# Performance work log

Hardware: AMD Instinct MI355X
Metric: run time of the kernel (lower is better)

Reference implementation:

```python
import jax, jax.numpy as jnp
import numpy as np

N_NODES = 50000
N_EDGES = 1600000
N_PAIRS = 2000000
N_GRAPHS = 50
HEADS = 4
HID = 32
T_LIMIT = 1.0
NEG_SLOPE = 0.2
LN_EPS = 1e-5


def setup_inputs() -> dict:
    key = jax.random.key(0)
    ks = jax.random.split(key, 24)
    inp = {}
    inp['x'] = jax.random.normal(ks[0], (N_NODES, 128), jnp.float32)
    inp['t'] = jax.random.uniform(ks[1], (N_NODES,), jnp.float32)
    inp['edge_index'] = jax.random.randint(ks[2], (2, N_EDGES), 0, N_NODES, jnp.int32)
    inp['pair_index'] = jax.random.randint(ks[3], (2, N_PAIRS), 0, N_NODES, jnp.int32)
    inp['batch'] = jnp.sort(jax.random.randint(ks[4], (N_NODES,), 0, N_GRAPHS, jnp.int32))
    s = lambda *sh: 0.05
    inp['t_W'] = jax.random.normal(ks[5], (3, 256), jnp.float32) * 0.3
    inp['t_b'] = jax.random.normal(ks[6], (256,), jnp.float32) * 0.05
    inp['W0_l'] = jax.random.normal(ks[7], (384, HEADS * HID), jnp.float32) * 0.05
    inp['b0_l'] = jax.random.normal(ks[8], (HEADS * HID,), jnp.float32) * 0.05
    inp['W0_r'] = jax.random.normal(ks[9], (384, HEADS * HID), jnp.float32) * 0.05
    inp['b0_r'] = jax.random.normal(ks[10], (HEADS * HID,), jnp.float32) * 0.05
    inp['att0'] = jax.random.normal(ks[11], (HEADS, HID), jnp.float32) * 0.1
    inp['bias0'] = jax.random.normal(ks[12], (HEADS * HID,), jnp.float32) * 0.05
    inp['Wl'] = jax.random.normal(ks[13], (3, HEADS * HID, HEADS * HID), jnp.float32) * 0.08
    inp['bl'] = jax.random.normal(ks[14], (3, HEADS * HID), jnp.float32) * 0.05
    inp['Wr'] = jax.random.normal(ks[15], (3, HEADS * HID, HEADS * HID), jnp.float32) * 0.08
    inp['br'] = jax.random.normal(ks[16], (3, HEADS * HID), jnp.float32) * 0.05
    inp['att'] = jax.random.normal(ks[17], (3, HEADS, HID), jnp.float32) * 0.1
    inp['bias'] = jax.random.normal(ks[18], (3, HEADS * HID), jnp.float32) * 0.05
    inp['ln_w'] = jnp.ones((4, HEADS * HID), jnp.float32)
    inp['ln_b'] = jnp.zeros((4, HEADS * HID), jnp.float32)
    inp['link_W'] = jax.random.normal(ks[19], (HEADS * HID, 1), jnp.float32) * 0.1
    inp['link_b'] = jnp.zeros((1,), jnp.float32)
    return inp


def gatv2_layer(h, src, dst, Wl_, bl_, Wr_, br_, att_, bias_):
    # GATv2Conv (concat heads, add_self_loops already folded into src/dst)
    n = h.shape[0]
    xl = (h @ Wl_ + bl_).reshape(n, HEADS, HID)   # source transform
    xr = (h @ Wr_ + br_).reshape(n, HEADS, HID)   # target transform
    m = jax.nn.leaky_relu(xl[src] + xr[dst], NEG_SLOPE)      # [E,H,C]
    logits = jnp.einsum('ehc,hc->eh', m, att_)               # [E,H]
    lmax = jax.ops.segment_max(logits, dst, num_segments=n)
    lmax = jnp.where(jnp.isfinite(lmax), lmax, 0.0)
    e = jnp.exp(logits - lmax[dst])
    denom = jax.ops.segment_sum(e, dst, num_segments=n)
    alpha = e / (denom[dst] + 1e-16)                         # scatter-softmax
    out = jax.ops.segment_sum(alpha[:, :, None] * xl[src], dst, num_segments=n)
    return out.reshape(n, HEADS * HID) + bias_


def graph_layernorm(h, batch, w, b):
    # PyG LayerNorm, mode='graph': normalize over all nodes+channels per graph
    n, f = h.shape
    cnt = jax.ops.segment_sum(jnp.ones((n,), h.dtype), batch, num_segments=N_GRAPHS) * f
    cnt = jnp.maximum(cnt, 1.0)
    mean = jax.ops.segment_sum(h.sum(axis=1), batch, num_segments=N_GRAPHS) / cnt
    hc = h - mean[batch][:, None]
    var = jax.ops.segment_sum((hc * hc).sum(axis=1), batch, num_segments=N_GRAPHS) / cnt
    return hc / jnp.sqrt(var + LN_EPS)[batch][:, None] * w + b


def reference(x, t, edge_index, pair_index, batch, t_W, t_b, W0_l, b0_l, W0_r, b0_r,
              att0, bias0, Wl, bl, Wr, br, att, bias, ln_w, ln_b, link_W, link_b):
    n = x.shape[0]
    # time embedding MLP with swish
    ta = (t / T_LIMIT)[:, None]
    feats = jnp.concatenate([jnp.sin(ta * (np.pi / 2)), jnp.cos(ta * (np.pi / 2)), ta], axis=1)
    te = feats @ t_W + t_b
    te = te * jax.nn.sigmoid(te)
    h = jnp.concatenate([x, te], axis=1)  # [N, 384]
    # self loops (added by GATv2Conv each layer)
    loops = jnp.arange(n, dtype=edge_index.dtype)
    src = jnp.concatenate([edge_index[0], loops])
    dst = jnp.concatenate([edge_index[1], loops])
    h = gatv2_layer(h, src, dst, W0_l, b0_l, W0_r, b0_r, att0, bias0)
    h = graph_layernorm(h, batch, ln_w[0], ln_b[0])
    for i in range(3):
        h = gatv2_layer(h, src, dst, Wl[i], bl[i], Wr[i], br[i], att[i], bias[i])
        h = graph_layernorm(h, batch, ln_w[i + 1], ln_b[i + 1])
    # edge-gather link scoring
    prod = h[pair_index[0]] * h[pair_index[1]]          # [E_pairs, 128]
    return jax.nn.sigmoid(prod @ link_W + link_b)[:, 0]
```

## Files before the change

kernel.cpp:

```cpp
#include <hip/hip_runtime.h>
#include <hip/hip_bf16.h>
#include <hip/hip_fp16.h>

#define N_NODES 50000
#define N_EDGES 1600000
#define E_TOT   1650000
#define N_PAIRS 2000000
#define N_GRAPHS 50
#define SCAN_NB 196

typedef __attribute__((ext_vector_type(2))) _Float16 half2_t;
typedef __attribute__((ext_vector_type(4))) _Float16 half4_t;
typedef __attribute__((ext_vector_type(8))) _Float16 half8_t;
typedef __attribute__((ext_vector_type(4))) float floatx4;

union H8 { half8_t v; half2_t h2[4]; uint32_t u[4]; };

__global__ void k_time_embed(const float* __restrict__ x, const float* __restrict__ t,
                             const float* __restrict__ tW, const float* __restrict__ tb,
                             _Float16* __restrict__ h0h) {
    int i = blockIdx.x;
    int tid = threadIdx.x;
    float ta = t[i];
    float s = sinf(ta * 1.5707963267948966f);
    float c = cosf(ta * 1.5707963267948966f);
    if (tid < 128) h0h[(size_t)i*384 + tid] = (_Float16)x[(size_t)i*128 + tid];
    float v = s*tW[tid] + c*tW[256+tid] + ta*tW[512+tid] + tb[tid];
    float sw = v / (1.f + __expf(-v));
    h0h[(size_t)i*384 + 128 + tid] = (_Float16)sw;
}

__global__ void k_cvt_w(const float* __restrict__ Wl, const float* __restrict__ Wr,
                        const float* __restrict__ bl, const float* __restrict__ br,
                        int K, _Float16* __restrict__ WT, float* __restrict__ b2) {
    int idx = blockIdx.x*256 + threadIdx.x;
    if (idx < 256) b2[idx] = (idx < 128) ? bl[idx] : br[idx-128];
    if (idx >= 256*K) return;
    int n = idx / K, k = idx - n*K;
    float v = (n < 128) ? Wl[k*128 + n] : Wr[k*128 + (n-128)];
    WT[idx] = (_Float16)v;
}

__global__ void k_edge_hist(const int* __restrict__ ei, int* __restrict__ deg) {
    int e = blockIdx.x*256 + threadIdx.x;
    if (e >= E_TOT) return;
    int dst = (e < N_EDGES) ? ei[N_EDGES + e] : (e - N_EDGES);
    atomicAdd(&deg[dst], 1);
}

__global__ void k_goff(const int* __restrict__ batch, int* __restrict__ goff) {
    int i = blockIdx.x*256 + threadIdx.x;
    if (i >= N_NODES) return;
    int bi = batch[i];
    if (i == 0) {
        for (int g = 0; g <= bi; ++g) goff[g] = 0;
    } else {
        int bp = batch[i-1];
        for (int g = bp+1; g <= bi; ++g) goff[g] = i;
    }
    if (i == N_NODES-1) {
        for (int g = bi+1; g <= N_GRAPHS; ++g) goff[g] = N_NODES;
    }
}

__global__ void k_scan1(const int* __restrict__ deg, int* __restrict__ row_ptr,
                        int* __restrict__ bsums) {
    __shared__ int tmp[256];
    int tid = threadIdx.x;
    int i = blockIdx.x*256 + tid;
    int v = (i < N_NODES) ? deg[i] : 0;
    tmp[tid] = v; __syncthreads();
    for (int off = 1; off < 256; off <<= 1) {
        int tv = (tid >= off) ? tmp[tid-off] : 0;
        __syncthreads();
        tmp[tid] += tv;
        __syncthreads();
    }
    int inc = tmp[tid];
    if (i < N_NODES) row_ptr[i] = inc - v;
    if (tid == 255) bsums[blockIdx.x] = inc;
}

__global__ void k_scan2(int* __restrict__ bsums, int nb) {
    __shared__ int tmp[256];
    int tid = threadIdx.x;
    int v = (tid < nb) ? bsums[tid] : 0;
    tmp[tid] = v; __syncthreads();
    for (int off = 1; off < 256; off <<= 1) {
        int tv = (tid >= off) ? tmp[tid-off] : 0;
        __syncthreads();
        tmp[tid] += tv;
        __syncthreads();
    }
    bsums[tid] = tmp[tid] - v;
}

__global__ void k_scan3(int* __restrict__ row_ptr, const int* __restrict__ bsums,
                        int* __restrict__ cursor) {
    int i = blockIdx.x*256 + threadIdx.x;
    if (i < N_NODES) {
        int v = row_ptr[i] + bsums[blockIdx.x];
        row_ptr[i] = v;
        cursor[i] = v;
    }
    if (i == 0) row_ptr[N_NODES] = E_TOT;
}

__global__ void k_scatter(const int* __restrict__ ei, int* __restrict__ cursor,
                          int* __restrict__ csr_src) {
    int e = blockIdx.x*256 + threadIdx.x;
    if (e >= E_TOT) return;
    int src, dst;
    if (e < N_EDGES) { src = ei[e]; dst = ei[N_EDGES + e]; }
    else             { src = e - N_EDGES; dst = src; }
    int pos = atomicAdd(&cursor[dst], 1);
    csr_src[pos] = src;
}

template<int K>
__global__ __launch_bounds__(256) void k_gemm_mfma(
    const _Float16* __restrict__ Ah, const _Float16* __restrict__ WT,
    const float* __restrict__ b2,
    _Float16* __restrict__ xl_h, float* __restrict__ xr) {
    int wave = (blockIdx.x*256 + threadIdx.x) >> 6;
    int lane = threadIdx.x & 63;
    if (wave >= N_NODES/16) return;
    int m0 = wave * 16;
    int r16 = lane & 15, quad = lane >> 4;
    constexpr int KT = K / 32;
    half8_t afrag[KT];
    const _Float16* arow = Ah + (size_t)(m0 + r16)*K + quad*8;
    #pragma unroll
    for (int kt = 0; kt < KT; ++kt)
        afrag[kt] = *(const half8_t*)(arow + kt*32);
    #pragma unroll
    for (int nt = 0; nt < 16; ++nt) {
        floatx4 acc = {0.f, 0.f, 0.f, 0.f};
        const _Float16* brow = WT + (size_t)(nt*16 + r16)*K + quad*8;
        #pragma unroll
        for (int kt = 0; kt < KT; ++kt) {
            half8_t bfrag = *(const half8_t*)(brow + kt*32);
            acc = __builtin_amdgcn_mfma_f32_16x16x32_f16(afrag[kt], bfrag, acc, 0, 0, 0);
        }
        int col = nt*16 + r16;
        float bv = b2[col];
        if (nt < 8) {
            #pragma unroll
            for (int r = 0; r < 4; ++r)
                xl_h[(size_t)(m0 + quad*4 + r)*128 + col] = (_Float16)(acc[r] + bv);
        } else {
            #pragma unroll
            for (int r = 0; r < 4; ++r)
                xr[(size_t)(m0 + quad*4 + r)*128 + (col-128)] = acc[r] + bv;
        }
    }
}

__global__ __launch_bounds__(256) void k_gemm_ln_mfma(
    const float* __restrict__ hout, const int* __restrict__ batch,
    const int* __restrict__ goff, const float* __restrict__ gsum,
    const float* __restrict__ gsumsq, const float* __restrict__ lnw,
    const float* __restrict__ lnb, const _Float16* __restrict__ WT,
    const float* __restrict__ b2,
    _Float16* __restrict__ xl_h, float* __restrict__ xr) {
    int wave = (blockIdx.x*256 + threadIdx.x) >> 6;
    int lane = threadIdx.x & 63;
    if (wave >= N_NODES/16) return;
    int m0 = wave * 16;
    int r16 = lane & 15, quad = lane >> 4;
    int row = m0 + r16;
    int g = batch[row];
    float cnt = (float)(goff[g+1] - goff[g]) * 128.f;
    cnt = fmaxf(cnt, 1.f);
    float mean = gsum[g] / cnt;
    float var = gsumsq[g] / cnt - mean*mean;
    var = fmaxf(var, 0.f);
    float rstd = rsqrtf(var + 1e-5f);

    half8_t afrag[4];
    const float* arow = hout + (size_t)row*128 + quad*8;
    #pragma unroll
    for (int kt = 0; kt < 4; ++kt) {
        int c = quad*8 + kt*32;
        const float4* v4 = (const float4*)(arow + kt*32);
        const float4* w4 = (const float4*)(lnw + c);
        const float4* b4 = (const float4*)(lnb + c);
        float4 v0 = v4[0], v1 = v4[1];
        float4 w0 = w4[0], w1 = w4[1];
        float4 bb0 = b4[0], bb1 = b4[1];
        float vv[8] = {v0.x,v0.y,v0.z,v0.w,v1.x,v1.y,v1.z,v1.w};
        float ww[8] = {w0.x,w0.y,w0.z,w0.w,w1.x,w1.y,w1.z,w1.w};
        float bz[8] = {bb0.x,bb0.y,bb0.z,bb0.w,bb1.x,bb1.y,bb1.z,bb1.w};
        #pragma unroll
        for (int j = 0; j < 8; ++j)
            afrag[kt][j] = (_Float16)((vv[j] - mean) * rstd * ww[j] + bz[j]);
    }
    #pragma unroll
    for (int nt = 0; nt < 16; ++nt) {
        floatx4 acc = {0.f, 0.f, 0.f, 0.f};
        const _Float16* brow = WT + (size_t)(nt*16 + r16)*128 + quad*8;
        #pragma unroll
        for (int kt = 0; kt < 4; ++kt) {
            half8_t bfrag = *(const half8_t*)(brow + kt*32);
            acc = __builtin_amdgcn_mfma_f32_16x16x32_f16(afrag[kt], bfrag, acc, 0, 0, 0);
        }
        int col = nt*16 + r16;
        float bv = b2[col];
        if (nt < 8) {
            #pragma unroll
            for (int r = 0; r < 4; ++r)
                xl_h[(size_t)(m0 + quad*4 + r)*128 + col] = (_Float16)(acc[r] + bv);
        } else {
            #pragma unroll
            for (int r = 0; r < 4; ++r)
                xr[(size_t)(m0 + quad*4 + r)*128 + (col-128)] = acc[r] + bv;
        }
    }
}

__global__ __launch_bounds__(256) void k_gat(
    const _Float16* __restrict__ xl_h, const float* __restrict__ xr,
    const int* __restrict__ row_ptr, const int* __restrict__ csr_src,
    const float* __restrict__ att, const float* __restrict__ bias,
    float* __restrict__ hout, float2* __restrict__ nstats) {
    int wave = (blockIdx.x * 256 + threadIdx.x) >> 6;
    int lane = threadIdx.x & 63;
    if (wave >= N_NODES) return;
    int i = wave;
    int slot = lane >> 4;
    int l16  = lane & 15;
    int c0   = l16 * 8;

    H8 atth, xrh;
    {
        const float4* a4 = (const float4*)(att + c0);
        const float4* r4 = (const float4*)(xr + (size_t)i*128 + c0);
        float4 a0 = a4[0], a1 = a4[1], r0 = r4[0], r1 = r4[1];
        float af[8] = {a0.x,a0.y,a0.z,a0.w,a1.x,a1.y,a1.z,a1.w};
        float rf[8] = {r0.x,r0.y,r0.z,r0.w,r1.x,r1.y,r1.z,r1.w};
        #pragma unroll
        for (int j = 0; j < 8; ++j) {
            atth.v[j] = (_Float16)af[j];
            xrh.v[j]  = (_Float16)rf[j];
        }
    }
    int p0 = row_ptr[i], p1 = row_ptr[i+1];

    float denom = 0.f;
    float acc[8];
    #pragma unroll
    for (int j = 0; j < 8; ++j) acc[j] = 0.f;

    for (int p = p0; p < p1; p += 8) {
        int e1 = p + slot, e2 = p + 4 + slot;
        int i1 = csr_src[(e1 < p1) ? e1 : (p1 - 1)];
        int i2 = csr_src[(e2 < p1) ? e2 : (p1 - 1)];
        H8 g1, g2, m1, m2;
        g1.v = *(const half8_t*)(xl_h + (size_t)i1*128 + c0);
        g2.v = *(const half8_t*)(xl_h + (size_t)i2*128 + c0);
        m1.v = g1.v + xrh.v;
        m2.v = g2.v + xrh.v;
        float pa1 = 0.f, pb1 = 0.f, pa2 = 0.f, pb2 = 0.f;
        #pragma unroll
        for (int j = 0; j < 4; ++j) {
            half2_t ab1 = __builtin_bit_cast(half2_t, m1.u[j] & 0x7FFF7FFFu);
            half2_t ab2 = __builtin_bit_cast(half2_t, m2.u[j] & 0x7FFF7FFFu);
            pa1 = __builtin_amdgcn_fdot2(m1.h2[j], atth.h2[j], pa1, false);
            pb1 = __builtin_amdgcn_fdot2(ab1,      atth.h2[j], pb1, false);
            pa2 = __builtin_amdgcn_fdot2(m2.h2[j], atth.h2[j], pa2, false);
            pb2 = __builtin_amdgcn_fdot2(ab2,      atth.h2[j], pb2, false);
        }
        float pt1 = 0.6f*pa1 + 0.4f*pb1;
        float pt2 = 0.6f*pa2 + 0.4f*pb2;
        pt1 += __shfl_xor(pt1, 1);  pt2 += __shfl_xor(pt2, 1);
        pt1 += __shfl_xor(pt1, 2);  pt2 += __shfl_xor(pt2, 2);
        float w1 = (e1 < p1) ? __expf(pt1) : 0.f;
        float w2 = (e2 < p1) ? __expf(pt2) : 0.f;
        denom += w1 + w2;
        #pragma unroll
        for (int j = 0; j < 8; ++j) {
            acc[j] = fmaf(w1, (float)g1.v[j], acc[j]);
            acc[j] = fmaf(w2, (float)g2.v[j], acc[j]);
        }
    }
    #pragma unroll
    for (int off = 16; off <= 32; off <<= 1) {
        denom += __shfl_xor(denom, off);
        #pragma unroll
        for (int j = 0; j < 8; ++j) acc[j] += __shfl_xor(acc[j], off);
    }
    float inv = 1.f / (denom + 1e-16f);
    float v[8];
    float s1 = 0.f, s2 = 0.f;
    #pragma unroll
    for (int j = 0; j < 8; ++j) {
        v[j] = acc[j] * inv + bias[c0 + j];
        s1 += v[j];
        s2 = fmaf(v[j], v[j], s2);
    }
    if (slot == 0) {
        float4* o4 = (float4*)(hout + (size_t)i*128 + c0);
        o4[0] = make_float4(v[0], v[1], v[2], v[3]);
        o4[1] = make_float4(v[4], v[5], v[6], v[7]);
    }
    #pragma unroll
    for (int off = 1; off < 16; off <<= 1) {
        s1 += __shfl_xor(s1, off);
        s2 += __shfl_xor(s2, off);
    }
    if (lane == 0) nstats[i] = make_float2(s1, s2);
}

__global__ __launch_bounds__(256) void k_graph_red(
    const float2* __restrict__ nstats, const int* __restrict__ goff,
    float* __restrict__ gsum, float* __restrict__ gsumsq) {
    __shared__ float l1[256], l2[256];
    int g = blockIdx.x;
    int tid = threadIdx.x;
    int a = goff[g], b = goff[g+1];
    float s1 = 0.f, s2 = 0.f;
    for (int i = a + tid; i < b; i += 256) {
        float2 v = nstats[i];
        s1 += v.x; s2 += v.y;
    }
    l1[tid] = s1; l2[tid] = s2; __syncthreads();
    for (int off = 128; off > 0; off >>= 1) {
        if (tid < off) { l1[tid] += l1[tid+off]; l2[tid] += l2[tid+off]; }
        __syncthreads();
    }
    if (tid == 0) { gsum[g] = l1[0]; gsumsq[g] = l2[0]; }
}

__global__ void k_ln(const float* __restrict__ hout, const int* __restrict__ batch,
                     const int* __restrict__ goff, const float* __restrict__ gsum,
                     const float* __restrict__ gsumsq, const float* __restrict__ w,
                     const float* __restrict__ b, _Float16* __restrict__ hb) {
    int idx = blockIdx.x*256 + threadIdx.x;
    if (idx >= N_NODES*128) return;
    int i = idx >> 7, c = idx & 127;
    int g = batch[i];
    float cnt = (float)(goff[g+1] - goff[g]) * 128.f;
    cnt = fmaxf(cnt, 1.f);
    float mean = gsum[g] / cnt;
    float var = gsumsq[g] / cnt - mean*mean;
    var = fmaxf(var, 0.f);
    float rstd = rsqrtf(var + 1e-5f);
    float v = (hout[idx] - mean) * rstd * w[c] + b[c];
    hb[idx] = (_Float16)v;
}

__global__ __launch_bounds__(256) void k_pairs(
    const _Float16* __restrict__ hb, const int* __restrict__ pi,
    const float* __restrict__ lW, const float* __restrict__ lb,
    float* __restrict__ out) {
    int grp = (blockIdx.x*256 + threadIdx.x) >> 4;
    int q = threadIdx.x & 15;
    if (grp >= N_PAIRS) return;
    H8 w;
    #pragma unroll
    for (int j = 0; j < 8; ++j) w.v[j] = (_Float16)lW[q*8 + j];
    int p0 = pi[grp], p1 = pi[N_PAIRS + grp];
    const half8_t* B = (const half8_t*)hb;
    H8 a, b, prod;
    a.v = B[(size_t)p0*16 + q];
    b.v = B[(size_t)p1*16 + q];
    prod.v = a.v * b.v;
    float part = 0.f;
    #pragma unroll
    for (int j = 0; j < 4; ++j)
        part = __builtin_amdgcn_fdot2(prod.h2[j], w.h2[j], part, false);
    part += __shfl_xor(part, 1);
    part += __shfl_xor(part, 2);
    part += __shfl_xor(part, 4);
    part += __shfl_xor(part, 8);
    if (q == 0) out[grp] = 1.f / (1.f + __expf(-(part + lb[0])));
}

extern "C" void kernel_launch(void* const* d_in, const int* in_sizes, int n_in,
                              void* d_out, int out_size, void* d_ws, size_t ws_size,
                              hipStream_t stream) {
    const float* x     = (const float*)d_in[0];
    const float* t     = (const float*)d_in[1];
    const int*   ei    = (const int*)  d_in[2];
    const int*   pi    = (const int*)  d_in[3];
    const int*   batch = (const int*)  d_in[4];
    const float* tW    = (const float*)d_in[5];
    const float* tb    = (const float*)d_in[6];
    const float* W0l   = (const float*)d_in[7];
    const float* b0l   = (const float*)d_in[8];
    const float* W0r   = (const float*)d_in[9];
    const float* b0r   = (const float*)d_in[10];
    const float* att0  = (const float*)d_in[11];
    const float* bias0 = (const float*)d_in[12];
    const float* Wl    = (const float*)d_in[13];
    const float* bl    = (const float*)d_in[14];
    const float* Wr    = (const float*)d_in[15];
    const float* br    = (const float*)d_in[16];
    const float* att   = (const float*)d_in[17];
    const float* bias  = (const float*)d_in[18];
    const float* lnw   = (const float*)d_in[19];
    const float* lnb   = (const float*)d_in[20];
    const float* lW    = (const float*)d_in[21];
    const float* lb    = (const float*)d_in[22];
    float* out = (float*)d_out;

    char* ws = (char*)d_ws;
    size_t off = 0;
    auto walloc = [&](size_t bytes) -> void* {
        void* p = ws + off;
        off += (bytes + 255) & ~(size_t)255;
        return p;
    };
    _Float16*  h0h     = (_Float16*) walloc((size_t)N_NODES*384*2);
    float*     hout    = (float*)    walloc((size_t)N_NODES*128*4);
    _Float16*  xl_h    = (_Float16*) walloc((size_t)N_NODES*128*2);
    float*     xr      = (float*)    walloc((size_t)N_NODES*128*4);
    _Float16*  hb      = (_Float16*) walloc((size_t)N_NODES*128*2);
    int*       deg     = (int*)      walloc((size_t)N_NODES*4);
    int*       row_ptr = (int*)      walloc((size_t)(N_NODES+1)*4);
    int*       csr_src = (int*)      walloc((size_t)E_TOT*4);
    int*       bsums   = (int*)      walloc(256*4);
    int*       goff    = (int*)      walloc(64*4);
    float2*    nstats  = (float2*)   walloc((size_t)N_NODES*8);
    float*     stats   = (float*)    walloc(2*64*4);
    _Float16*  WT0     = (_Float16*) walloc(256*384*2);
    _Float16*  WT123   = (_Float16*) walloc(3*256*128*2);
    float*     b2      = (float*)    walloc(4*256*4);

    hipMemsetAsync(deg, 0, (size_t)N_NODES*4, stream);

    k_time_embed<<<N_NODES, 256, 0, stream>>>(x, t, tW, tb, h0h);
    k_cvt_w<<<(256*384+255)/256, 256, 0, stream>>>(W0l, W0r, b0l, b0r, 384, WT0, b2);
    for (int l = 0; l < 3; ++l)
        k_cvt_w<<<(256*128+255)/256, 256, 0, stream>>>(
            Wl + (size_t)l*128*128, Wr + (size_t)l*128*128,
            bl + l*128, br + l*128, 128, WT123 + (size_t)l*256*128, b2 + (l+1)*256);
    k_edge_hist<<<(E_TOT+255)/256, 256, 0, stream>>>(ei, deg);
    k_goff<<<SCAN_NB, 256, 0, stream>>>(batch, goff);
    k_scan1<<<SCAN_NB, 256, 0, stream>>>(deg, row_ptr, bsums);
    k_scan2<<<1, 256, 0, stream>>>(bsums, SCAN_NB);
    k_scan3<<<SCAN_NB, 256, 0, stream>>>(row_ptr, bsums, deg);
    k_scatter<<<(E_TOT+255)/256, 256, 0, stream>>>(ei, deg, csr_src);

    float* gsum   = stats;
    float* gsumsq = stats + 64;
    const int GEMM_BLOCKS = (N_NODES/16 + 3) / 4;
    for (int L = 0; L < 4; ++L) {
        if (L == 0)
            k_gemm_mfma<384><<<GEMM_BLOCKS, 256, 0, stream>>>(h0h, WT0, b2, xl_h, xr);
        else
            k_gemm_ln_mfma<<<GEMM_BLOCKS, 256, 0, stream>>>(
                hout, batch, goff, gsum, gsumsq, lnw + (L-1)*128, lnb + (L-1)*128,
                WT123 + (size_t)(L-1)*256*128, b2 + L*256, xl_h, xr);
        const float* attL  = (L == 0) ? att0  : att  + (size_t)(L-1)*128;
        const float* biasL = (L == 0) ? bias0 : bias + (size_t)(L-1)*128;
        k_gat<<<N_NODES/4, 256, 0, stream>>>(xl_h, xr, row_ptr, csr_src, attL, biasL,
                                             hout, nstats);
        k_graph_red<<<N_GRAPHS, 256, 0, stream>>>(nstats, goff, gsum, gsumsq);
    }
    k_ln<<<(N_NODES*128+255)/256, 256, 0, stream>>>(hout, batch, goff, gsum, gsumsq,
                                                    lnw + 3*128, lnb + 3*128, hb);
    k_pairs<<<((size_t)N_PAIRS*16 + 255)/256, 256, 0, stream>>>(hb, pi, lW, lb, out);
}
```

Baseline: 959.0 us.

## Replace global-atomic CSR build with two-pass bucketed scatter in shared memory

The CSR construction moves from a global per-node degree histogram plus scan plus global-atomic scatter to a two-level bucket sort. Edges are first binned into 256 buckets of 196 destination nodes using shared-memory histograms. A second pass sorts each bucket locally and writes row_ptr and csr_src with shared-memory atomics only. This is meant to cut global atomic contention and scattered writes, at the cost of an extra staging buffer and an additional read of the edge list. The packed stage word holds src in 16 bits, and source ids up to 49999 fit in that.

Result: faster. 821.3 us (-14.4%).

```diff
diff --git a/kernel.cpp b/kernel.cpp
--- a/kernel.cpp
+++ b/kernel.cpp
@@ -8,6 +8,9 @@
 #define N_PAIRS 2000000
 #define N_GRAPHS 50
 #define SCAN_NB 196
+#define NB2 256
+#define BSZ 196
+#define SCAT_BLOCKS 256
 
 typedef __attribute__((ext_vector_type(2))) _Float16 half2_t;
 typedef __attribute__((ext_vector_type(4))) _Float16 half4_t;
@@ -41,13 +44,6 @@
     WT[idx] = (_Float16)v;
 }
 
-__global__ void k_edge_hist(const int* __restrict__ ei, int* __restrict__ deg) {
-    int e = blockIdx.x*256 + threadIdx.x;
-    if (e >= E_TOT) return;
-    int dst = (e < N_EDGES) ? ei[N_EDGES + e] : (e - N_EDGES);
-    atomicAdd(&deg[dst], 1);
-}
-
 __global__ void k_goff(const int* __restrict__ batch, int* __restrict__ goff) {
     int i = blockIdx.x*256 + threadIdx.x;
     if (i >= N_NODES) return;
@@ -63,58 +59,105 @@
     }
 }
 
-__global__ void k_scan1(const int* __restrict__ deg, int* __restrict__ row_ptr,
-                        int* __restrict__ bsums) {
-    __shared__ int tmp[256];
+__global__ __launch_bounds__(256) void k_bhist(const int* __restrict__ ei,
+                                               int* __restrict__ bcnt) {
+    __shared__ int lh[NB2];
     int tid = threadIdx.x;
-    int i = blockIdx.x*256 + tid;
-    int v = (i < N_NODES) ? deg[i] : 0;
+    lh[tid] = 0;
+    __syncthreads();
+    int chunk = (E_TOT + gridDim.x - 1) / gridDim.x;
+    int e0 = blockIdx.x * chunk;
+    int e1 = min(e0 + chunk, E_TOT);
+    for (int e = e0 + tid; e < e1; e += 256) {
+        int dst = (e < N_EDGES) ? ei[N_EDGES + e] : (e - N_EDGES);
+        atomicAdd(&lh[dst / BSZ], 1);
+    }
+    __syncthreads();
+    if (lh[tid]) atomicAdd(&bcnt[tid], lh[tid]);
+}
+
+__global__ void k_bscan(const int* __restrict__ bcnt, int* __restrict__ bbase,
+                        int* __restrict__ bcursor) {
+    __shared__ int tmp[NB2];
+    int tid = threadIdx.x;
+    int v = bcnt[tid];
     tmp[tid] = v; __syncthreads();
-    for (int off = 1; off < 256; off <<= 1) {
-        int tv = (tid >= off) ? tmp[tid-off] : 0;
+    for (int off = 1; off < NB2; off <<= 1) {
+        int t = (tid >= off) ? tmp[tid-off] : 0;
         __syncthreads();
-        tmp[tid] += tv;
+        tmp[tid] += t;
         __syncthreads();
     }
-    int inc = tmp[tid];
-    if (i < N_NODES) row_ptr[i] = inc - v;
-    if (tid == 255) bsums[blockIdx.x] = inc;
-}
-
-__global__ void k_scan2(int* __restrict__ bsums, int nb) {
-    __shared__ int tmp[256];
+    int excl = tmp[tid] - v;
+    bbase[tid] = excl;
+    bcursor[tid] = excl;
+    if (tid == NB2-1) bbase[NB2] = tmp[tid];
+}
+
+__global__ __launch_bounds__(256) void k_scat1(const int* __restrict__ ei,
+                                               int* __restrict__ bcursor,
+                                               unsigned int* __restrict__ stage) {
+    __shared__ int lh[NB2];
+    __shared__ int lpos[NB2];
     int tid = threadIdx.x;
-    int v = (tid < nb) ? bsums[tid] : 0;
-    tmp[tid] = v; __syncthreads();
-    for (int off = 1; off < 256; off <<= 1) {
-        int tv = (tid >= off) ? tmp[tid-off] : 0;
+    lh[tid] = 0;
+    __syncthreads();
+    int chunk = (E_TOT + gridDim.x - 1) / gridDim.x;
+    int e0 = blockIdx.x * chunk;
+    int e1 = min(e0 + chunk, E_TOT);
+    for (int e = e0 + tid; e < e1; e += 256) {
+        int dst = (e < N_EDGES) ? ei[N_EDGES + e] : (e - N_EDGES);
+        atomicAdd(&lh[dst / BSZ], 1);
+    }
+    __syncthreads();
+    int cnt = lh[tid];
+    lpos[tid] = cnt ? atomicAdd(&bcursor[tid], cnt) : 0;
+    __syncthreads();
+    for (int e = e0 + tid; e < e1; e += 256) {
+        int src, dst;
+        if (e < N_EDGES) { src = ei[e]; dst = ei[N_EDGES + e]; }
+        else             { src = e - N_EDGES; dst = src; }
+        int b = dst / BSZ;
+        int dl = dst - b * BSZ;
+        int pos = atomicAdd(&lpos[b], 1);
+        stage[pos] = ((unsigned int)dl << 16) | (unsigned int)src;
+    }
+}
+
+__global__ __launch_bounds__(256) void k_scat2(
+    const unsigned int* __restrict__ stage, const int* __restrict__ bbase,
+    int* __restrict__ row_ptr, int* __restrict__ csr_src) {
+    __shared__ int hist[NB2];
+    __shared__ int cur[NB2];
+    int b = blockIdx.x;
+    int tid = threadIdx.x;
+    hist[tid] = 0;
+    __syncthreads();
+    int p0 = bbase[b], p1 = bbase[b+1];
+    for (int p = p0 + tid; p < p1; p += 256)
+        atomicAdd(&hist[stage[p] >> 16], 1);
+    __syncthreads();
+    int v = hist[tid];
+    cur[tid] = v; __syncthreads();
+    for (int off = 1; off < NB2; off <<= 1) {
+        int t = (tid >= off) ? cur[tid-off] : 0;
         __syncthreads();
-        tmp[tid] += tv;
+        cur[tid] += t;
         __syncthreads();
     }
-    bsums[tid] = tmp[tid] - v;
-}
-
-__global__ void k_scan3(int* __restrict__ row_ptr, const int* __restrict__ bsums,
-                        int* __restrict__ cursor) {
-    int i = blockIdx.x*256 + threadIdx.x;
-    if (i < N_NODES) {
-        int v = row_ptr[i] + bsums[blockIdx.x];
-        row_ptr[i] = v;
-        cursor[i] = v;
-    }
-    if (i == 0) row_ptr[N_NODES] = E_TOT;
-}
-
-__global__ void k_scatter(const int* __restrict__ ei, int* __restrict__ cursor,
-                          int* __restrict__ csr_src) {
-    int e = blockIdx.x*256 + threadIdx.x;
-    if (e >= E_TOT) return;
-    int src, dst;
-    if (e < N_EDGES) { src = ei[e]; dst = ei[N_EDGES + e]; }
-    else             { src = e - N_EDGES; dst = src; }
-    int pos = atomicAdd(&cursor[dst], 1);
-    csr_src[pos] = src;
+    int excl = cur[tid] - v;
+    int node = b*BSZ + tid;
+    if (tid < BSZ && node < N_NODES) row_ptr[node] = p0 + excl;
+    __syncthreads();
+    cur[tid] = p0 + excl;
+    __syncthreads();
+    for (int p = p0 + tid; p < p1; p += 256) {
+        unsigned int u = stage[p];
+        int dl = (int)(u >> 16);
+        int pos = atomicAdd(&cur[dl], 1);
+        csr_src[pos] = (int)(u & 0xFFFFu);
+    }
+    if (b == NB2-1 && tid == 0) row_ptr[N_NODES] = E_TOT;
 }
 
 template<int K>
@@ -416,10 +459,12 @@
     _Float16*  xl_h    = (_Float16*) walloc((size_t)N_NODES*128*2);
     float*     xr      = (float*)    walloc((size_t)N_NODES*128*4);
     _Float16*  hb      = (_Float16*) walloc((size_t)N_NODES*128*2);
-    int*       deg     = (int*)      walloc((size_t)N_NODES*4);
     int*       row_ptr = (int*)      walloc((size_t)(N_NODES+1)*4);
     int*       csr_src = (int*)      walloc((size_t)E_TOT*4);
-    int*       bsums   = (int*)      walloc(256*4);
+    unsigned int* stage = (unsigned int*)walloc((size_t)E_TOT*4);
+    int*       bcnt    = (int*)      walloc(NB2*4);
+    int*       bbase   = (int*)      walloc((NB2+1)*4);
+    int*       bcursor = (int*)      walloc(NB2*4);
     int*       goff    = (int*)      walloc(64*4);
     float2*    nstats  = (float2*)   walloc((size_t)N_NODES*8);
     float*     stats   = (float*)    walloc(2*64*4);
@@ -427,7 +472,7 @@
     _Float16*  WT123   = (_Float16*) walloc(3*256*128*2);
     float*     b2      = (float*)    walloc(4*256*4);
 
-    hipMemsetAsync(deg, 0, (size_t)N_NODES*4, stream);
+    hipMemsetAsync(bcnt, 0, NB2*4, stream);
 
     k_time_embed<<<N_NODES, 256, 0, stream>>>(x, t, tW, tb, h0h);
     k_cvt_w<<<(256*384+255)/256, 256, 0, stream>>>(W0l, W0r, b0l, b0r, 384, WT0, b2);
@@ -435,12 +480,11 @@
         k_cvt_w<<<(256*128+255)/256, 256, 0, stream>>>(
             Wl + (size_t)l*128*128, Wr + (size_t)l*128*128,
             bl + l*128, br + l*128, 128, WT123 + (size_t)l*256*128, b2 + (l+1)*256);
-    k_edge_hist<<<(E_TOT+255)/256, 256, 0, stream>>>(ei, deg);
     k_goff<<<SCAN_NB, 256, 0, stream>>>(batch, goff);
-    k_scan1<<<SCAN_NB, 256, 0, stream>>>(deg, row_ptr, bsums);
-    k_scan2<<<1, 256, 0, stream>>>(bsums, SCAN_NB);
-    k_scan3<<<SCAN_NB, 256, 0, stream>>>(row_ptr, bsums, deg);
-    k_scatter<<<(E_TOT+255)/256, 256, 0, stream>>>(ei, deg, csr_src);
+    k_bhist<<<SCAT_BLOCKS, 256, 0, stream>>>(ei, bcnt);
+    k_bscan<<<1, 256, 0, stream>>>(bcnt, bbase, bcursor);
+    k_scat1<<<SCAT_BLOCKS, 256, 0, stream>>>(ei, bcursor, stage);
+    k_scat2<<<NB2, 256, 0, stream>>>(stage, bbase, row_ptr, csr_src);
 
     float* gsum   = stats;
     float* gsumsq = stats + 64;
```
